# Optimization experiments

Hardware: AMD Instinct MI355X
Metric: run time of the kernel (lower is better)

The kernel has to match this reference:

```python
import jax, jax.numpy as jnp
import numpy as np

N_NODES = 100000


def add_self_loops(edge_index, num_nodes):
    loops = jnp.arange(num_nodes, dtype=edge_index.dtype)
    src = jnp.concatenate([edge_index[0], loops])
    dst = jnp.concatenate([edge_index[1], loops])
    return src, dst


def gcn_conv(x, src, dst, W, b, num_nodes):
    # symmetric normalization D^-1/2 A_hat D^-1/2 (A_hat includes self-loops)
    ones = jnp.ones(dst.shape[0], dtype=x.dtype)
    deg = jax.ops.segment_sum(ones, dst, num_segments=num_nodes)
    dinv = jnp.where(deg > 0, jax.lax.rsqrt(deg), 0.0)
    norm = dinv[src] * dinv[dst]                      # [E+N]
    h = x @ W                                         # [N, out]
    msg = h[src] * norm[:, None]                      # gather + scale
    out = jax.ops.segment_sum(msg, dst, num_segments=num_nodes)  # scatter-add
    return out + b


def setup_inputs() -> dict:
    key = jax.random.key(0)
    k1, k2, k3, k4 = jax.random.split(key, 4)
    N, C, H, E = N_NODES, 256, 64, 1600000
    x = jax.random.normal(k1, (N, C), dtype=jnp.float32)
    edge_index = jax.random.randint(k2, (2, E), 0, N, dtype=jnp.int64)
    # xavier_uniform init as in the torch module
    lim1 = float(np.sqrt(6.0 / (C + H)))
    lim2 = float(np.sqrt(6.0 / (H + C)))
    W1 = jax.random.uniform(k3, (C, H), dtype=jnp.float32, minval=-lim1, maxval=lim1)
    W2 = jax.random.uniform(k4, (H, C), dtype=jnp.float32, minval=-lim2, maxval=lim2)
    b1 = jnp.zeros((H,), dtype=jnp.float32)
    b2 = jnp.zeros((C,), dtype=jnp.float32)
    return {"x": x, "edge_index": edge_index, "W1": W1, "b1": b1, "W2": W2, "b2": b2}


def reference(x, edge_index, W1, b1, W2, b2):
    N = x.shape[0]
    src, dst = add_self_loops(edge_index, N)
    h = gcn_conv(x, src, dst, W1, b1, N)
    h = jax.nn.relu(h)
    # dropout is identity at inference (eval mode)
    h = gcn_conv(h, src, dst, W2, b2, N)
    return jnp.tanh(h)
```

## Files before the change

### kernel.cpp

```cpp
#include <hip/hip_runtime.h>
#include <math.h>

#define CIN 256
#define HD  64

__global__ __launch_bounds__(256) void k_hist(const int* __restrict__ dst,
                                              int* __restrict__ deg, int E) {
  int e = blockIdx.x * 256 + threadIdx.x;
  if (e < E) atomicAdd(&deg[dst[e]], 1);
}

__global__ __launch_bounds__(256) void k_dinv2(const int* __restrict__ deg,
                                               float* __restrict__ dinv, int N) {
  int i = blockIdx.x * 256 + threadIdx.x;
  if (i < N) dinv[i] = rsqrtf((float)deg[i] + 1.0f);
}

__global__ __launch_bounds__(256) void k_scan1(const int* __restrict__ deg,
                                               int* __restrict__ rowstart,
                                               int* __restrict__ partials, int N) {
  __shared__ int sh[256];
  int g = blockIdx.x * 256 + threadIdx.x;
  int v = (g < N) ? deg[g] : 0;
  sh[threadIdx.x] = v;
  __syncthreads();
  int acc = v;
  for (int off = 1; off < 256; off <<= 1) {
    int t = 0;
    if ((int)threadIdx.x >= off) t = sh[threadIdx.x - off];
    __syncthreads();
    acc += t;
    sh[threadIdx.x] = acc;
    __syncthreads();
  }
  if (g < N) rowstart[g] = acc - v;
  if (threadIdx.x == 255) partials[blockIdx.x] = acc;
}

__global__ __launch_bounds__(512) void k_scan2(int* __restrict__ partials, int nblk) {
  if (nblk > 512) {
    if (threadIdx.x == 0) {
      int run = 0;
      for (int i = 0; i < nblk; ++i) { int t = partials[i]; partials[i] = run; run += t; }
    }
    return;
  }
  __shared__ int sh[512];
  int v = ((int)threadIdx.x < nblk) ? partials[threadIdx.x] : 0;
  sh[threadIdx.x] = v;
  __syncthreads();
  int acc = v;
  for (int off = 1; off < 512; off <<= 1) {
    int t = 0;
    if ((int)threadIdx.x >= off) t = sh[threadIdx.x - off];
    __syncthreads();
    acc += t;
    sh[threadIdx.x] = acc;
    __syncthreads();
  }
  if ((int)threadIdx.x < nblk) partials[threadIdx.x] = acc - v;
}

__global__ __launch_bounds__(256) void k_scan3(int* __restrict__ rowstart,
                                               const int* __restrict__ partials, int N) {
  int g = blockIdx.x * 256 + threadIdx.x;
  if (g < N) rowstart[g] += partials[blockIdx.x];
}

__global__ __launch_bounds__(256) void k_fill(const int* __restrict__ src,
                                              const int* __restrict__ dst,
                                              const int* __restrict__ rowstart,
                                              int* __restrict__ fill,
                                              int* __restrict__ csr, int E) {
  int e = blockIdx.x * 256 + threadIdx.x;
  if (e < E) {
    int d = dst[e];
    int p = atomicAdd(&fill[d], 1);
    csr[rowstart[d] + p] = src[e];
  }
}

__global__ __launch_bounds__(256) void k_agg(const int* __restrict__ rowstart,
                                             const int* __restrict__ deg,
                                             const int* __restrict__ csr,
                                             const float* __restrict__ hs,
                                             float* __restrict__ acc, int N) {
  int t = blockIdx.x * 256 + threadIdx.x;
  int n = t >> 4;
  if (n >= N) return;
  int qc = t & 15;
  const float4* hp = (const float4*)hs;
  float4 a = hp[(size_t)n * 16 + qc];
  int r0 = rowstart[n], dg = deg[n];
  for (int i = 0; i < dg; ++i) {
    int s = csr[r0 + i];
    float4 v = hp[(size_t)s * 16 + qc];
    a.x += v.x; a.y += v.y; a.z += v.z; a.w += v.w;
  }
  ((float4*)acc)[(size_t)n * 16 + qc] = a;
}

#define FMA4(ar, xs, wv)            \
  ar[0] = fmaf(xs, wv.x, ar[0]);    \
  ar[1] = fmaf(xs, wv.y, ar[1]);    \
  ar[2] = fmaf(xs, wv.z, ar[2]);    \
  ar[3] = fmaf(xs, wv.w, ar[3]);

__global__ __launch_bounds__(256) void k_gemm1(const float* __restrict__ x,
                                               const float* __restrict__ W1,
                                               const float* __restrict__ dinv,
                                               float* __restrict__ hs,
                                               float* __restrict__ acc, int N) {
  __shared__ float Wl[CIN * HD];
  int tid = threadIdx.x;
#pragma unroll
  for (int i = 0; i < (CIN * HD) / 256; ++i) Wl[tid + i * 256] = W1[tid + i * 256];
  __syncthreads();

  int tn = tid >> 4, tj = tid & 15;
  int n0 = blockIdx.x * 64 + tn * 4;
  int j0 = tj * 4;

  const float* xp0 = x + (size_t)(n0 + 0 < N ? n0 + 0 : N - 1) * CIN;
  const float* xp1 = x + (size_t)(n0 + 1 < N ? n0 + 1 : N - 1) * CIN;
  const float* xp2 = x + (size_t)(n0 + 2 < N ? n0 + 2 : N - 1) * CIN;
  const float* xp3 = x + (size_t)(n0 + 3 < N ? n0 + 3 : N - 1) * CIN;

  float a[4][4] = {};
  for (int c = 0; c < CIN; c += 4) {
    float4 w0 = *(const float4*)&Wl[(c + 0) * HD + j0];
    float4 w1 = *(const float4*)&Wl[(c + 1) * HD + j0];
    float4 w2 = *(const float4*)&Wl[(c + 2) * HD + j0];
    float4 w3 = *(const float4*)&Wl[(c + 3) * HD + j0];
    float4 x0 = *(const float4*)(xp0 + c);
    float4 x1 = *(const float4*)(xp1 + c);
    float4 x2 = *(const float4*)(xp2 + c);
    float4 x3 = *(const float4*)(xp3 + c);
    FMA4(a[0], x0.x, w0); FMA4(a[0], x0.y, w1); FMA4(a[0], x0.z, w2); FMA4(a[0], x0.w, w3);
    FMA4(a[1], x1.x, w0); FMA4(a[1], x1.y, w1); FMA4(a[1], x1.z, w2); FMA4(a[1], x1.w, w3);
    FMA4(a[2], x2.x, w0); FMA4(a[2], x2.y, w1); FMA4(a[2], x2.z, w2); FMA4(a[2], x2.w, w3);
    FMA4(a[3], x3.x, w0); FMA4(a[3], x3.y, w1); FMA4(a[3], x3.z, w2); FMA4(a[3], x3.w, w3);
  }

#pragma unroll
  for (int i = 0; i < 4; ++i) {
    int n = n0 + i;
    if (n < N) {
      float dv = dinv[n];
      float4 v = make_float4(a[i][0] * dv, a[i][1] * dv, a[i][2] * dv, a[i][3] * dv);
      *(float4*)&hs[(size_t)n * HD + j0]  = v;
      *(float4*)&acc[(size_t)n * HD + j0] = v;
    }
  }
}

__global__ __launch_bounds__(256) void k_scatter(const int* __restrict__ src,
                                                 const int* __restrict__ dst,
                                                 const float* __restrict__ hs,
                                                 float* __restrict__ acc, int E) {
  int t = blockIdx.x * 256 + threadIdx.x;
  int e = t >> 4;
  if (e < E) {
    int q = (t & 15) * 4;
    int s = src[e], d = dst[e];
    float4 v = *(const float4*)&hs[(size_t)s * HD + q];
    float* p = &acc[(size_t)d * HD + q];
    atomicAdd(p + 0, v.x);
    atomicAdd(p + 1, v.y);
    atomicAdd(p + 2, v.z);
    atomicAdd(p + 3, v.w);
  }
}

__global__ __launch_bounds__(256) void k_deg(const int* __restrict__ dst,
                                             float* __restrict__ deg, int E) {
  int e = blockIdx.x * 256 + threadIdx.x;
  if (e < E) atomicAdd(&deg[dst[e]], 1.0f);
}
__global__ __launch_bounds__(256) void k_dinv(float* __restrict__ deg, int N) {
  int i = blockIdx.x * 256 + threadIdx.x;
  if (i < N) deg[i] = rsqrtf(deg[i] + 1.0f);
}

__global__ __launch_bounds__(256) void k_fin1(const float* __restrict__ b1,
                                              const float* __restrict__ dinv,
                                              float* __restrict__ acc,
                                              float* __restrict__ hs, int N64) {
  int t = blockIdx.x * 256 + threadIdx.x;
  if (t < N64) {
    int n = t >> 6, j = t & 63;
    float dv = dinv[n];
    float v = fmaf(acc[t], dv, b1[j]);
    v = fmaxf(v, 0.0f);
    v *= dv;
    hs[t] = v;
    acc[t] = v;
  }
}

__device__ inline float fast_tanh(float v) {
  v = fminf(fmaxf(v, -15.0f), 15.0f);
  float e2 = __expf(2.0f * v);
  return (e2 - 1.0f) * __builtin_amdgcn_rcpf(e2 + 1.0f);
}

__global__ __launch_bounds__(256) void k_gemm2(const float* __restrict__ acc2,
                                               const float* __restrict__ W2,
                                               const float* __restrict__ dinv,
                                               const float* __restrict__ b2,
                                               float* __restrict__ out, int N) {
  __shared__ float Wl[HD * 64];
  int tid = threadIdx.x;
  int cb = blockIdx.y * 64;
#pragma unroll
  for (int i = 0; i < (HD * 64) / 256; ++i) {
    int idx = tid + i * 256;
    Wl[idx] = W2[(idx >> 6) * 256 + cb + (idx & 63)];
  }
  __syncthreads();

  int tn = tid >> 4, tj = tid & 15;
  int n0 = blockIdx.x * 64 + tn * 4;
  int j0 = tj * 4;

  const float* hp0 = acc2 + (size_t)(n0 + 0 < N ? n0 + 0 : N - 1) * HD;
  const float* hp1 = acc2 + (size_t)(n0 + 1 < N ? n0 + 1 : N - 1) * HD;
  const float* hp2 = acc2 + (size_t)(n0 + 2 < N ? n0 + 2 : N - 1) * HD;
  const float* hp3 = acc2 + (size_t)(n0 + 3 < N ? n0 + 3 : N - 1) * HD;

  float a[4][4] = {};
  for (int k = 0; k < HD; k += 4) {
    float4 w0 = *(const float4*)&Wl[(k + 0) * 64 + j0];
    float4 w1 = *(const float4*)&Wl[(k + 1) * 64 + j0];
    float4 w2 = *(const float4*)&Wl[(k + 2) * 64 + j0];
    float4 w3 = *(const float4*)&Wl[(k + 3) * 64 + j0];
    float4 x0 = *(const float4*)(hp0 + k);
    float4 x1 = *(const float4*)(hp1 + k);
    float4 x2 = *(const float4*)(hp2 + k);
    float4 x3 = *(const float4*)(hp3 + k);
    FMA4(a[0], x0.x, w0); FMA4(a[0], x0.y, w1); FMA4(a[0], x0.z, w2); FMA4(a[0], x0.w, w3);
    FMA4(a[1], x1.x, w0); FMA4(a[1], x1.y, w1); FMA4(a[1], x1.z, w2); FMA4(a[1], x1.w, w3);
    FMA4(a[2], x2.x, w0); FMA4(a[2], x2.y, w1); FMA4(a[2], x2.z, w2); FMA4(a[2], x2.w, w3);
    FMA4(a[3], x3.x, w0); FMA4(a[3], x3.y, w1); FMA4(a[3], x3.z, w2); FMA4(a[3], x3.w, w3);
  }

#pragma unroll
  for (int i = 0; i < 4; ++i) {
    int n = n0 + i;
    if (n < N) {
      float dv = dinv[n];
      float4 r;
      r.x = fast_tanh(fmaf(a[i][0], dv, b2[cb + j0 + 0]));
      r.y = fast_tanh(fmaf(a[i][1], dv, b2[cb + j0 + 1]));
      r.z = fast_tanh(fmaf(a[i][2], dv, b2[cb + j0 + 2]));
      r.w = fast_tanh(fmaf(a[i][3], dv, b2[cb + j0 + 3]));
      *(float4*)&out[(size_t)n * 256 + cb + j0] = r;
    }
  }
}

extern "C" void kernel_launch(void* const* d_in, const int* in_sizes, int n_in,
                              void* d_out, int out_size, void* d_ws, size_t ws_size,
                              hipStream_t stream) {
  const float* x  = (const float*)d_in[0];
  const int*   ei = (const int*)d_in[1];
  const float* W1 = (const float*)d_in[2];
  const float* b1 = (const float*)d_in[3];
  const float* W2 = (const float*)d_in[4];
  const float* b2 = (const float*)d_in[5];
  float* out = (float*)d_out;

  int N = in_sizes[0] / CIN;
  int E = in_sizes[1] / 2;
  const int* src = ei;
  const int* dst = ei + E;

  auto align256 = [](size_t v) { return (v + 255) & ~(size_t)255; };
  size_t nb  = align256((size_t)N * 4);
  size_t eb  = align256((size_t)E * 4);
  size_t fb  = align256((size_t)N * HD * 4);

  size_t need = nb * 4 + align256(512 * 4) + eb + fb * 2;

  char* ws = (char*)d_ws;
  int nblk = (N + 255) / 256;

  if (ws_size >= need) {
    float* dinv     = (float*)ws;
    int*   deg      = (int*)(ws + nb);
    int*   rowstart = (int*)(ws + nb * 2);
    int*   fillc    = (int*)(ws + nb * 3);
    int*   partials = (int*)(ws + nb * 4);
    int*   csr      = (int*)(ws + nb * 4 + align256(512 * 4));
    float* bufA     = (float*)(ws + nb * 4 + align256(512 * 4) + eb);
    float* bufB     = bufA + (size_t)N * HD;

    hipMemsetAsync(deg,   0, (size_t)N * 4, stream);
    hipMemsetAsync(fillc, 0, (size_t)N * 4, stream);
    k_hist <<<(E + 255) / 256, 256, 0, stream>>>(dst, deg, E);
    k_dinv2<<<nblk, 256, 0, stream>>>(deg, dinv, N);
    k_scan1<<<nblk, 256, 0, stream>>>(deg, rowstart, partials, N);
    k_scan2<<<1, 512, 0, stream>>>(partials, nblk);
    k_scan3<<<nblk, 256, 0, stream>>>(rowstart, partials, N);
    k_fill <<<(E + 255) / 256, 256, 0, stream>>>(src, dst, rowstart, fillc, csr, E);

    k_gemm1<<<(N + 63) / 64, 256, 0, stream>>>(x, W1, dinv, bufA, bufB, N);
    k_agg  <<<((size_t)N * 16 + 255) / 256, 256, 0, stream>>>(rowstart, deg, csr, bufA, bufB, N);
    k_fin1 <<<((size_t)N * HD + 255) / 256, 256, 0, stream>>>(b1, dinv, bufB, bufA, N * HD);
    k_agg  <<<((size_t)N * 16 + 255) / 256, 256, 0, stream>>>(rowstart, deg, csr, bufA, bufB, N);
    dim3 g2((N + 63) / 64, 4);
    k_gemm2<<<g2, 256, 0, stream>>>(bufB, W2, dinv, b2, out, N);
  } else {
    float* dinv = (float*)ws;
    float* bufA = (float*)(ws + nb);
    float* bufB = bufA + (size_t)N * HD;

    hipMemsetAsync(dinv, 0, (size_t)N * 4, stream);
    k_deg <<<(E + 255) / 256, 256, 0, stream>>>(dst, dinv, E);
    k_dinv<<<nblk, 256, 0, stream>>>(dinv, N);
    k_gemm1<<<(N + 63) / 64, 256, 0, stream>>>(x, W1, dinv, bufA, bufB, N);
    k_scatter<<<((size_t)E * 16 + 255) / 256, 256, 0, stream>>>(src, dst, bufA, bufB, E);
    k_fin1<<<((size_t)N * HD + 255) / 256, 256, 0, stream>>>(b1, dinv, bufB, bufA, N * HD);
    k_scatter<<<((size_t)E * 16 + 255) / 256, 256, 0, stream>>>(src, dst, bufA, bufB, E);
    dim3 g2((N + 63) / 64, 4);
    k_gemm2<<<g2, 256, 0, stream>>>(bufB, W2, dinv, b2, out, N);
  }
}
```

Baseline: 607.0 us.

## Fuse bias/ReLU/normalization into aggregation, halve GEMM1 LDS tile, drop redundant acc write

Folds the layer-1 finalize (bias, ReLU, dinv scaling) into the first CSR aggregation's epilogue, removing a separate elementwise kernel and a full N×64 round trip. GEMM1 stops writing the duplicate acc buffer on the CSR path and stages W1 in two 128-row halves, cutting LDS from 64KB to 32KB to allow more resident blocks. The aggregation loop prefetches the next neighbor index before the gather to shorten the dependent load chain. The buffer ping-pong is rearranged so GEMM2 reads the second aggregation's result.

```diff
diff --git a/kernel.cpp b/kernel.cpp
--- a/kernel.cpp
+++ b/kernel.cpp
@@ -80,11 +80,14 @@
   }
 }
 
+template <bool FUSE>
 __global__ __launch_bounds__(256) void k_agg(const int* __restrict__ rowstart,
                                              const int* __restrict__ deg,
                                              const int* __restrict__ csr,
                                              const float* __restrict__ hs,
-                                             float* __restrict__ acc, int N) {
+                                             float* __restrict__ outb,
+                                             const float* __restrict__ dinv,
+                                             const float* __restrict__ b1, int N) {
   int t = blockIdx.x * 256 + threadIdx.x;
   int n = t >> 4;
   if (n >= N) return;
@@ -92,12 +95,26 @@
   const float4* hp = (const float4*)hs;
   float4 a = hp[(size_t)n * 16 + qc];
   int r0 = rowstart[n], dg = deg[n];
-  for (int i = 0; i < dg; ++i) {
-    int s = csr[r0 + i];
+  if (dg > 0) {
+    int s = csr[r0];
+    for (int i = 1; i < dg; ++i) {
+      int s_next = csr[r0 + i];
+      float4 v = hp[(size_t)s * 16 + qc];
+      a.x += v.x; a.y += v.y; a.z += v.z; a.w += v.w;
+      s = s_next;
+    }
     float4 v = hp[(size_t)s * 16 + qc];
     a.x += v.x; a.y += v.y; a.z += v.z; a.w += v.w;
   }
-  ((float4*)acc)[(size_t)n * 16 + qc] = a;
+  if (FUSE) {
+    float dv = dinv[n];
+    float4 bb = *(const float4*)&b1[qc * 4];
+    a.x = fmaxf(fmaf(a.x, dv, bb.x), 0.0f) * dv;
+    a.y = fmaxf(fmaf(a.y, dv, bb.y), 0.0f) * dv;
+    a.z = fmaxf(fmaf(a.z, dv, bb.z), 0.0f) * dv;
+    a.w = fmaxf(fmaf(a.w, dv, bb.w), 0.0f) * dv;
+  }
+  ((float4*)outb)[(size_t)n * 16 + qc] = a;
 }
 
 #define FMA4(ar, xs, wv)            \
@@ -110,13 +127,10 @@
                                                const float* __restrict__ W1,
                                                const float* __restrict__ dinv,
                                                float* __restrict__ hs,
-                                               float* __restrict__ acc, int N) {
-  __shared__ float Wl[CIN * HD];
+                                               float* __restrict__ acc, int N,
+                                               int write_acc) {
+  __shared__ float Wl[128 * HD];
   int tid = threadIdx.x;
-#pragma unroll
-  for (int i = 0; i < (CIN * HD) / 256; ++i) Wl[tid + i * 256] = W1[tid + i * 256];
-  __syncthreads();
-
   int tn = tid >> 4, tj = tid & 15;
   int n0 = blockIdx.x * 64 + tn * 4;
   int j0 = tj * 4;
@@ -127,19 +141,28 @@
   const float* xp3 = x + (size_t)(n0 + 3 < N ? n0 + 3 : N - 1) * CIN;
 
   float a[4][4] = {};
-  for (int c = 0; c < CIN; c += 4) {
-    float4 w0 = *(const float4*)&Wl[(c + 0) * HD + j0];
-    float4 w1 = *(const float4*)&Wl[(c + 1) * HD + j0];
-    float4 w2 = *(const float4*)&Wl[(c + 2) * HD + j0];
-    float4 w3 = *(const float4*)&Wl[(c + 3) * HD + j0];
-    float4 x0 = *(const float4*)(xp0 + c);
-    float4 x1 = *(const float4*)(xp1 + c);
-    float4 x2 = *(const float4*)(xp2 + c);
-    float4 x3 = *(const float4*)(xp3 + c);
-    FMA4(a[0], x0.x, w0); FMA4(a[0], x0.y, w1); FMA4(a[0], x0.z, w2); FMA4(a[0], x0.w, w3);
-    FMA4(a[1], x1.x, w0); FMA4(a[1], x1.y, w1); FMA4(a[1], x1.z, w2); FMA4(a[1], x1.w, w3);
-    FMA4(a[2], x2.x, w0); FMA4(a[2], x2.y, w1); FMA4(a[2], x2.z, w2); FMA4(a[2], x2.w, w3);
-    FMA4(a[3], x3.x, w0); FMA4(a[3], x3.y, w1); FMA4(a[3], x3.z, w2); FMA4(a[3], x3.w, w3);
+#pragma unroll
+  for (int kh = 0; kh < 2; ++kh) {
+#pragma unroll
+    for (int i = 0; i < (128 * HD) / 256; ++i)
+      Wl[tid + i * 256] = W1[kh * 128 * HD + tid + i * 256];
+    __syncthreads();
+    int cbase = kh * 128;
+    for (int c = 0; c < 128; c += 4) {
+      float4 w0 = *(const float4*)&Wl[(c + 0) * HD + j0];
+      float4 w1 = *(const float4*)&Wl[(c + 1) * HD + j0];
+      float4 w2 = *(const float4*)&Wl[(c + 2) * HD + j0];
+      float4 w3 = *(const float4*)&Wl[(c + 3) * HD + j0];
+      float4 x0 = *(const float4*)(xp0 + cbase + c);
+      float4 x1 = *(const float4*)(xp1 + cbase + c);
+      float4 x2 = *(const float4*)(xp2 + cbase + c);
+      float4 x3 = *(const float4*)(xp3 + cbase + c);
+      FMA4(a[0], x0.x, w0); FMA4(a[0], x0.y, w1); FMA4(a[0], x0.z, w2); FMA4(a[0], x0.w, w3);
+      FMA4(a[1], x1.x, w0); FMA4(a[1], x1.y, w1); FMA4(a[1], x1.z, w2); FMA4(a[1], x1.w, w3);
+      FMA4(a[2], x2.x, w0); FMA4(a[2], x2.y, w1); FMA4(a[2], x2.z, w2); FMA4(a[2], x2.w, w3);
+      FMA4(a[3], x3.x, w0); FMA4(a[3], x3.y, w1); FMA4(a[3], x3.z, w2); FMA4(a[3], x3.w, w3);
+    }
+    __syncthreads();
   }
 
 #pragma unroll
@@ -148,8 +171,8 @@
     if (n < N) {
       float dv = dinv[n];
       float4 v = make_float4(a[i][0] * dv, a[i][1] * dv, a[i][2] * dv, a[i][3] * dv);
-      *(float4*)&hs[(size_t)n * HD + j0]  = v;
-      *(float4*)&acc[(size_t)n * HD + j0] = v;
+      *(float4*)&hs[(size_t)n * HD + j0] = v;
+      if (write_acc) *(float4*)&acc[(size_t)n * HD + j0] = v;
     }
   }
 }
@@ -276,9 +299,9 @@
   const int* dst = ei + E;
 
   auto align256 = [](size_t v) { return (v + 255) & ~(size_t)255; };
-  size_t nb  = align256((size_t)N * 4);
-  size_t eb  = align256((size_t)E * 4);
-  size_t fb  = align256((size_t)N * HD * 4);
+  size_t nb = align256((size_t)N * 4);
+  size_t eb = align256((size_t)E * 4);
+  size_t fb = align256((size_t)N * HD * 4);
 
   size_t need = nb * 4 + align256(512 * 4) + eb + fb * 2;
 
@@ -304,12 +327,12 @@
     k_scan3<<<nblk, 256, 0, stream>>>(rowstart, partials, N);
     k_fill <<<(E + 255) / 256, 256, 0, stream>>>(src, dst, rowstart, fillc, csr, E);
 
-    k_gemm1<<<(N + 63) / 64, 256, 0, stream>>>(x, W1, dinv, bufA, bufB, N);
-    k_agg  <<<((size_t)N * 16 + 255) / 256, 256, 0, stream>>>(rowstart, deg, csr, bufA, bufB, N);
-    k_fin1 <<<((size_t)N * HD + 255) / 256, 256, 0, stream>>>(b1, dinv, bufB, bufA, N * HD);
-    k_agg  <<<((size_t)N * 16 + 255) / 256, 256, 0, stream>>>(rowstart, deg, csr, bufA, bufB, N);
+    size_t aggGrid = ((size_t)N * 16 + 255) / 256;
+    k_gemm1<<<(N + 63) / 64, 256, 0, stream>>>(x, W1, dinv, bufA, bufB, N, 0);
+    k_agg<true> <<<aggGrid, 256, 0, stream>>>(rowstart, deg, csr, bufA, bufB, dinv, b1, N);
+    k_agg<false><<<aggGrid, 256, 0, stream>>>(rowstart, deg, csr, bufB, bufA, dinv, b1, N);
     dim3 g2((N + 63) / 64, 4);
-    k_gemm2<<<g2, 256, 0, stream>>>(bufB, W2, dinv, b2, out, N);
+    k_gemm2<<<g2, 256, 0, stream>>>(bufA, W2, dinv, b2, out, N);
   } else {
     float* dinv = (float*)ws;
     float* bufA = (float*)(ws + nb);
@@ -318,7 +341,7 @@
     hipMemsetAsync(dinv, 0, (size_t)N * 4, stream);
     k_deg <<<(E + 255) / 256, 256, 0, stream>>>(dst, dinv, E);
     k_dinv<<<nblk, 256, 0, stream>>>(dinv, N);
-    k_gemm1<<<(N + 63) / 64, 256, 0, stream>>>(x, W1, dinv, bufA, bufB, N);
+    k_gemm1<<<(N + 63) / 64, 256, 0, stream>>>(x, W1, dinv, bufA, bufB, N, 1);
     k_scatter<<<((size_t)E * 16 + 255) / 256, 256, 0, stream>>>(src, dst, bufA, bufB, E);
     k_fin1<<<((size_t)N * HD + 255) / 256, 256, 0, stream>>>(b1, dinv, bufB, bufA, N * HD);
     k_scatter<<<((size_t)E * 16 + 255) / 256, 256, 0, stream>>>(src, dst, bufA, bufB, E);
```

Measured after the change: 571.9 us. 5.8% less time.
